# Kernel tuning notes

Hardware: AMD Instinct MI355X
Metric: run time of the kernel (lower is better)

Reference implementation:

```python
import jax, jax.numpy as jnp
import numpy as np

B, T, F = 256, 2048, 20
H_NODES = 256


def _heaviside(x):
    # smooth heaviside approx used throughout the original module
    return (jnp.tanh(10.0 * x) + 1.0) * 0.5


def _evap(wu, wl, wd, pet):
    h = _heaviside
    et1 = h(wu - pet) * pet + h(pet - wu) * wu
    rp = h(pet - et1) * (pet - et1)  # h(-(pet-et1))*0 term vanishes
    et22 = h(rp - wl) * wl + h(wl - rp) * rp
    et2 = h(rp) * et22
    et33 = h(rp - et2 - wd) * wd + h(wd - (rp - et2)) * (rp - et2)
    et3 = h(rp - et2) * et33
    return et1, et2, et3


def _runoff(wu, wl, wd, p, wum, wlm, wdm, b, c):
    wum = wum * 19.9 + 0.1
    wlm = wlm * 30.0 + 60.0
    wdm = wdm * 60.0 + 60.0
    c = c * 0.19 + 0.01
    b = b * 0.3 + 0.1
    w_total = wum + wlm + wdm
    s = c * (wu / w_total) ** 2 + b * (wl / w_total) ** 2
    return _heaviside(p - s) * (p - s)


def _partition(runoff, k1, k2, k3):
    k1 = k1 * 0.69 + 0.01
    k2 = k2 * 0.69 + 0.01
    k3 = k3 * 0.89 + 0.01
    sr = k1 * runoff
    itf = k2 * (runoff - sr)
    bf = k3 * (runoff - sr - itf)
    return sr, itf, bf


def setup_inputs() -> dict:
    key = jax.random.key(0)
    ks = jax.random.split(key, 7)
    u = lambda k, shp: jax.random.uniform(k, shp, jnp.float32, -0.05, 0.05)
    inputs = jax.random.uniform(ks[0], (B, T, F), jnp.float32)
    return {
        "inputs": inputs,
        "w1": u(ks[1], (15, H_NODES)),
        "b1": jnp.zeros((H_NODES,), jnp.float32),
        "w2": u(ks[2], (H_NODES, 64)),
        "b2": jnp.zeros((64,), jnp.float32),
        "w3": u(ks[3], (64, 8)),
        "b3": jnp.zeros((8,), jnp.float32),
    }


def reference(inputs, w1, b1, w2, b2, w3, b3):
    pet = inputs[..., 0:1]
    tmean = inputs[..., 1:2]
    p = inputs[..., 2:3]
    attrs = inputs[..., 5:]  # [B,T,15]

    # static-attribute -> physical-parameter MLP
    h1 = jnp.tanh(attrs @ w1 + b1)
    h2 = jnp.tanh(h1 @ w2 + b2)
    params = jax.nn.sigmoid(h2 @ w3 + b3)  # [B,T,8]

    xs = jnp.concatenate([pet, p, tmean, params], axis=-1)  # [B,T,11]

    def step(state, x):
        wu, wl, wd = state[:, 0:1], state[:, 1:2], state[:, 2:3]
        pet_t, p_t = x[:, 0:1], x[:, 1:2]
        et1, et2, et3 = _evap(wu, wl, wd, pet_t)
        clip = lambda d: jnp.clip(d, -1e5, 1e5)
        wu_n = wu + clip(p_t - et1)
        wl_n = wl + clip(p_t - et1 - et2)
        wd_n = wd + clip(p_t - et1 - et2 - et3)
        ns = jnp.concatenate([wu_n, wl_n, wd_n], axis=1)  # [B,3]
        return ns, ns

    init = jnp.zeros((inputs.shape[0], 3), inputs.dtype)
    _, outs = jax.lax.scan(step, init, jnp.swapaxes(xs, 0, 1))  # [T,B,3]
    outputs = jnp.swapaxes(outs, 0, 1)  # [B,T,3]

    wu, wl, wd = outputs[..., 0:1], outputs[..., 1:2], outputs[..., 2:3]
    wum, wlm, wdm = params[..., 0:1], params[..., 1:2], params[..., 2:3]
    b, c = params[..., 3:4], params[..., 4:5]
    k1, k2, k3 = params[..., 5:6], params[..., 6:7], params[..., 7:8]

    et1, et2, et3 = _evap(wu, wl, wd, pet)
    # NOTE: original call() swaps (wl,wd) and (wlm,wdm) here - kept faithful
    runoff = _runoff(wu, wd, wl, p, wum, wdm, wlm, b, c)
    sr, itf, bf = _partition(runoff, k1, k2, k3)
    total_q = sr + itf * 0.5 + bf * 0.25  # flow routing
    return total_q  # [B,T,1]
```

## Files before the change

### kernel.cpp

```cpp
#include <hip/hip_runtime.h>

#define B_ 256
#define T_ 2048
#define F_ 20
#define NT (B_*T_)

typedef __bf16 bf16x8 __attribute__((ext_vector_type(8)));
typedef float  f32x4  __attribute__((ext_vector_type(4)));

__device__ __forceinline__ float ex2(float x){ return __builtin_amdgcn_exp2f(x); }
__device__ __forceinline__ float rcpf_(float x){ return __builtin_amdgcn_rcpf(x); }

#define K10F 28.853900817779268f
#define K1F   2.8853900817779268f
#define LOG2E 1.4426950408889634f

__device__ __forceinline__ float hside(float x){ return 1.0f - rcpf_(ex2(K10F*x) + 1.0f); }
__device__ __forceinline__ float tanh_f(float z){ return 1.0f - 2.0f*rcpf_(ex2(K1F*z) + 1.0f); }
__device__ __forceinline__ float sigmoid_f(float z){ return rcpf_(1.0f + ex2(-LOG2E*z)); }


__global__ __launch_bounds__(256) void prep_kernel(const float* __restrict__ in,
                                                   float* __restrict__ ws){
  int r = blockIdx.x*256 + threadIdx.x;
  if (r >= NT) return;
  int b = r & (B_-1);
  int t = r >> 8;
  const float* src = in + ((size_t)b*T_ + t)*F_;
  ((float2*)ws)[r] = make_float2(src[0], src[2]);
}

__global__ __launch_bounds__(512) void fused_kernel(const float* __restrict__ in,
    const float* __restrict__ w1, const float* __restrict__ b1,
    const float* __restrict__ w2, const float* __restrict__ b2,
    const float* __restrict__ w3, const float* __restrict__ b3,
    float* __restrict__ ws){
  extern __shared__ char sm[];
  float* pk4 = ws + 4*(size_t)NT;

  if (blockIdx.x < 4) {
    asm volatile("s_setprio 3");
    const float2* pp2 = (const float2*)ws;
    float* wuT = ws + 2*(size_t)NT;
    float* wdT = ws + 3*(size_t)NT;
    float2* abL = (float2*)sm;
    float2* qbL = (float2*)(sm + 32768);

    int tid = threadIdx.x;
    int wv = tid >> 6, lane = tid & 63;
    int boff = blockIdx.x * 64;

    float wu = 0.0f, wl = 0.0f, wd = 0.0f;
    float2 buf[2][8];

    if (wv == 0){
      #pragma unroll
      for (int i = 0; i < 8; ++i){
        buf[0][i] = pp2[(    i)*B_ + boff + lane];
        buf[1][i] = pp2[(8 + i)*B_ + boff + lane];
      }
    }

    for (int it = 0; it < 66; ++it){
      if (wv == 0){
        if (it < 64){
          int c = it, par = c & 1;
          #pragma unroll
          for (int g = 0; g < 4; ++g){
            #pragma unroll
            for (int i = 0; i < 8; ++i){
              int s = g*8 + i;
              float pet = buf[g&1][i].x, p = buf[g&1][i].y;
              float d  = wu - pet;
              float r1 = rcpf_(ex2(K10F*d) + 1.0f);
              float d1 = -d*r1;
              float base = (p - pet) + d1;
              wu += base;
              wuT[(c*32 + s)*B_ + boff + lane] = wu;
              float r2 = rcpf_(ex2(K10F*d1) + 1.0f);
              float rp = fmaf(-d1, r2, d1);
              abL[(par*32 + s)*64 + lane] = make_float2(rp, base);
            }
            int gn = c*4 + g + 2;
            if (gn > 255) gn = 255;
            #pragma unroll
            for (int i = 0; i < 8; ++i)
              buf[g&1][i] = pp2[(gn*8 + i)*B_ + boff + lane];
          }
        }
      } else if (wv == 1){
        if (it >= 1 && it <= 64){
          int c = it - 1, par = c & 1;
          #pragma unroll 1
          for (int half = 0; half < 2; ++half){
            #pragma unroll
            for (int s0 = 0; s0 < 16; ++s0){
              int s = half*16 + s0;
              float2 ab  = abL[(par*32 + s)*64 + lane];
              float rp   = ab.x, base = ab.y;
              float hrp  = 1.0f - rcpf_(ex2(K10F*rp) + 1.0f);
              float d2   = rp - wl;
              float r    = rcpf_(ex2(K10F*d2) + 1.0f);
              float et22 = fmaf(d2, r, wl);
              float et2  = hrp * et22;
              float b2v  = base - et2;
              wl += b2v;
              qbL[(par*32 + s)*64 + lane] = make_float2(rp - et2, b2v);
            }
          }
        }
      } else if (wv == 2){
        if (it >= 2){
          int c = it - 2, par = c & 1;
          #pragma unroll 1
          for (int half = 0; half < 2; ++half){
            #pragma unroll
            for (int s0 = 0; s0 < 16; ++s0){
              int s = half*16 + s0;
              float2 qb  = qbL[(par*32 + s)*64 + lane];
              float hqv  = 1.0f - rcpf_(ex2(K10F*qb.x) + 1.0f);
              float d3   = qb.x - wd;
              float r    = rcpf_(ex2(K10F*d3) + 1.0f);
              float et33 = fmaf(d3, r, wd);
              float et3  = hqv * et33;
              wd += qb.y - et3;
              wdT[(c*32 + s)*B_ + boff + lane] = wd;
            }
          }
        }
      }
      __syncthreads();
    }
    return;
  }

  __bf16* w1f   = (__bf16*)sm;
  __bf16* w2f   = (__bf16*)(sm + 8192);
  float*  b1s   = (float*)(sm + 24576);
  float*  b2s   = (float*)(sm + 25600);
  float*  b3s   = (float*)(sm + 25856);
  __bf16* hbufA = (__bf16*)(sm + 25888);

  int tid  = threadIdx.x;
  int lane = tid & 63;
  int wv   = tid >> 6;
  int m    = lane & 15;
  int q    = lane >> 4;
  int r0   = (blockIdx.x - 4)*256 + wv*32;

  bf16x8 a1[2];
  #pragma unroll
  for (int u = 0; u < 2; ++u){
    int rowA = r0 + u*16 + m;
    int bA = rowA & (B_-1), tA = rowA >> 8;
    const float* ap = in + ((size_t)bA*T_ + tA)*F_ + 5;
    #pragma unroll
    for (int j = 0; j < 8; ++j){
      int k = q*8 + j;
      a1[u][j] = (__bf16)((k < 15) ? ap[k] : 0.0f);
    }
  }
  bf16x8 w3h[2], w3l[2];
  #pragma unroll
  for (int kb = 0; kb < 2; ++kb){
    #pragma unroll
    for (int j = 0; j < 8; ++j){
      float v = (m < 8) ? w3[(kb*32 + q*8 + j)*8 + m] : 0.0f;
      __bf16 hi = (__bf16)v;
      w3h[kb][j] = hi;
      w3l[kb][j] = (__bf16)(v - (float)hi);
    }
  }

  ((float4*)sm)[tid] = make_float4(0.0f, 0.0f, 0.0f, 0.0f);
  __syncthreads();
  for (int idx = tid; idx < 15*256; idx += 512){
    int k = idx >> 8, n = idx & 255;
    int ct = n >> 4;
    int l  = ((k>>3)*16) + (n & 15);
    int j  = k & 7;
    w1f[(ct*32 + l)*8 + j] = (__bf16)w1[idx];
  }
  for (int idx = tid; idx < 8192; idx += 512){
    int kk = idx >> 6, n = idx & 63;
    int kb2 = kk >> 5;
    int lq  = (kk >> 3) & 3;
    int j   = kk & 7;
    int ct  = n >> 4;
    int l   = lq*16 + (n & 15);
    w2f[((kb2*4 + ct)*64 + l)*8 + j] = (__bf16)w2[kk*64 + n];
  }
  if (tid < 256) b1s[tid] = b1[tid];
  if (tid < 64)  b2s[tid] = b2[tid];
  if (tid < 8)   b3s[tid] = b3[tid];
  __syncthreads();

  f32x4 zero4 = {0.0f, 0.0f, 0.0f, 0.0f};
  bf16x8 zero8;
  #pragma unroll
  for (int j = 0; j < 8; ++j) zero8[j] = (__bf16)0.0f;

  __bf16* hb = hbufA + wv*2304;
  f32x4 acc2[2][4] = {{zero4, zero4, zero4, zero4},
                      {zero4, zero4, zero4, zero4}};

  #pragma unroll
  for (int pc = 0; pc < 2; ++pc){
    if (pc == 1){
      __syncthreads();
      for (int idx = tid; idx < 8192; idx += 512){
        int kk = idx >> 6, n = idx & 63;
        int kb2 = kk >> 5;
        int lq  = (kk >> 3) & 3;
        int j   = kk & 7;
        int ct  = n >> 4;
        int l   = lq*16 + (n & 15);
        w2f[((kb2*4 + ct)*64 + l)*8 + j] = (__bf16)w2[(128 + kk)*64 + n];
      }
      __syncthreads();
    }
    #pragma unroll
    for (int ph = 0; ph < 2; ++ph){
      int p = pc*2 + ph;
      #pragma unroll
      for (int c4 = 0; c4 < 4; ++c4){
        int ct = p*4 + c4;
        bf16x8 bw = zero8;
        if (lane < 32) bw = *(const bf16x8*)&w1f[(ct*32 + lane)*8];
        int f = c4*16 + m;
        float bb = b1s[p*64 + f];
        #pragma unroll
        for (int u = 0; u < 2; ++u){
          f32x4 c1 = __builtin_amdgcn_mfma_f32_16x16x32_bf16(a1[u], bw, zero4, 0, 0, 0);
          #pragma unroll
          for (int i = 0; i < 4; ++i){
            float h = tanh_f(c1[i] + bb);
            hb[(u*16 + q*4 + i)*72 + f] = (__bf16)h;
          }
        }
      }
      #pragma unroll
      for (int kb = 0; kb < 2; ++kb){
        bf16x8 a2_0 = *(const bf16x8*)&hb[ m      *72 + kb*32 + q*8];
        bf16x8 a2_1 = *(const bf16x8*)&hb[(16 + m)*72 + kb*32 + q*8];
        #pragma unroll
        for (int ct = 0; ct < 4; ++ct){
          bf16x8 bw2 = *(const bf16x8*)&w2f[(((ph*2 + kb)*4 + ct)*64 + lane)*8];
          acc2[0][ct] = __builtin_amdgcn_mfma_f32_16x16x32_bf16(a2_0, bw2, acc2[0][ct], 0, 0, 0);
          acc2[1][ct] = __builtin_amdgcn_mfma_f32_16x16x32_bf16(a2_1, bw2, acc2[1][ct], 0, 0, 0);
        }
      }
    }
  }

  #pragma unroll
  for (int ct = 0; ct < 4; ++ct){
    int f = ct*16 + m;
    float bb = b2s[f];
    #pragma unroll
    for (int u = 0; u < 2; ++u)
      #pragma unroll
      for (int i = 0; i < 4; ++i){
        float h = tanh_f(acc2[u][ct][i] + bb);
        hb[(u*16 + q*4 + i)*72 + f] = (__bf16)h;
      }
  }

  f32x4 acc3[2] = {zero4, zero4};
  #pragma unroll
  for (int kb = 0; kb < 2; ++kb){
    bf16x8 a3_0 = *(const bf16x8*)&hb[ m      *72 + kb*32 + q*8];
    bf16x8 a3_1 = *(const bf16x8*)&hb[(16 + m)*72 + kb*32 + q*8];
    acc3[0] = __builtin_amdgcn_mfma_f32_16x16x32_bf16(a3_0, w3h[kb], acc3[0], 0, 0, 0);
    acc3[0] = __builtin_amdgcn_mfma_f32_16x16x32_bf16(a3_0, w3l[kb], acc3[0], 0, 0, 0);
    acc3[1] = __builtin_amdgcn_mfma_f32_16x16x32_bf16(a3_1, w3h[kb], acc3[1], 0, 0, 0);
    acc3[1] = __builtin_amdgcn_mfma_f32_16x16x32_bf16(a3_1, w3l[kb], acc3[1], 0, 0, 0);
  }

  float* hf = (float*)hb;
  if (m < 8){
    float bb3 = b3s[m];
    #pragma unroll
    for (int u = 0; u < 2; ++u)
      #pragma unroll
      for (int i = 0; i < 4; ++i)
        hf[(u*16 + q*4 + i)*9 + m] = sigmoid_f(acc3[u][i] + bb3);
  }
  if (lane < 32){
    const float* Pr = hf + lane*9;
    float P0=Pr[0], P1=Pr[1], P2=Pr[2], P3=Pr[3];
    float P4=Pr[4], P5=Pr[5], P6=Pr[6], P7=Pr[7];
    float wum = fmaf(P0, 19.9f, 0.1f);
    float wlm = fmaf(P2, 30.0f, 60.0f);
    float wdm = fmaf(P1, 60.0f, 60.0f);
    float wt  = wum + wlm + wdm;
    float rw  = 1.0f / wt;
    float cc  = fmaf(P4, 0.19f, 0.01f);
    float bc  = fmaf(P3, 0.30f, 0.10f);
    float A   = cc*rw*rw;
    float Bc  = bc*rw*rw;
    float k1  = fmaf(P5, 0.69f, 0.01f);
    float k2  = fmaf(P6, 0.69f, 0.01f);
    float k3  = fmaf(P7, 0.89f, 0.01f);
    float KP  = k1 + 0.5f*k2*(1.0f-k1) + 0.25f*k3*(1.0f-k1)*(1.0f-k2);
    *(float4*)&pk4[(size_t)(r0 + lane)*4] = make_float4(A, Bc, KP, 0.0f);
  }
}

__global__ __launch_bounds__(256) void final_kernel(const float* __restrict__ ws,
                                                    float* __restrict__ out){
  __shared__ float tile[64*65];
  int tb = blockIdx.x & 31;
  int bb = blockIdx.x >> 5;
  int t0 = tb*64, b0 = bb*64;
  int tid = threadIdx.x;
  const float2* pp2 = (const float2*)ws;
  const float* wuT  = ws + 2*(size_t)NT;
  const float* wdT  = ws + 3*(size_t)NT;
  const float* pk4  = ws + 4*(size_t)NT;

  #pragma unroll
  for (int k = 0; k < 16; ++k){
    int idx = k*256 + tid;
    int tl = idx >> 6, bl = idx & 63;
    int r = (t0 + tl)*B_ + b0 + bl;
    float p  = pp2[r].y;
    float wu = wuT[r], wd = wdT[r];
    float4 k4 = *(const float4*)&pk4[(size_t)r*4];
    float ps = p - k4.x*wu*wu - k4.y*wd*wd;
    float runoff = hside(ps)*ps;
    tile[bl*65 + tl] = k4.z * runoff;
  }
  __syncthreads();
  #pragma unroll
  for (int k = 0; k < 16; ++k){
    int idx = k*256 + tid;
    int tl2 = idx & 63, bl2 = idx >> 6;
    out[(size_t)(b0 + bl2)*T_ + t0 + tl2] = tile[bl2*65 + tl2];
  }
}

extern "C" void kernel_launch(void* const* d_in, const int* in_sizes, int n_in,
                              void* d_out, int out_size, void* d_ws, size_t ws_size,
                              hipStream_t stream) {
  const float* in = (const float*)d_in[0];
  const float* w1 = (const float*)d_in[1];
  const float* b1 = (const float*)d_in[2];
  const float* w2 = (const float*)d_in[3];
  const float* b2 = (const float*)d_in[4];
  const float* w3 = (const float*)d_in[5];
  const float* b3 = (const float*)d_in[6];
  float* out = (float*)d_out;
  float* ws  = (float*)d_ws;

  static bool attr_set = false;
  if (!attr_set){
    hipFuncSetAttribute((const void*)fused_kernel,
                        hipFuncAttributeMaxDynamicSharedMemorySize, 65536);
    attr_set = true;
  }

  prep_kernel <<<NT/256,     256, 0,     stream>>>(in, ws);
  fused_kernel<<<NT/256 + 4, 512, 65536, stream>>>(in, w1, b1, w2, b2, w3, b3, ws);
  final_kernel<<<128,        256, 0,     stream>>>(ws, out);
}
```

Baseline: 221.6 us.

## Move recurrent scan into prep kernel and read forcings directly from input

The sequential three-store scan moves out of the fused MLP kernel and into the prep kernel, as 4 extra blocks that run alongside the transpose blocks. The scan wave now loads pet and p straight from the original input with float4 loads and a deeper 4-group prefetch, instead of reading the transposed workspace. This removes the scan's dependence on the prep pass and frees the MLP kernel from hosting long-running scan blocks. The cost is that the scan no longer overlaps the MLP, which now starts only after the scan finishes. The per-lane loads are also strided across batch rows and poorly coalesced.

Result: slower. 388.0 us (+75.1%).

```diff
diff --git a/kernel.cpp b/kernel.cpp
--- a/kernel.cpp
+++ b/kernel.cpp
@@ -20,17 +20,113 @@
 __device__ __forceinline__ float sigmoid_f(float z){ return rcpf_(1.0f + ex2(-LOG2E*z)); }
 
 
-__global__ __launch_bounds__(256) void prep_kernel(const float* __restrict__ in,
-                                                   float* __restrict__ ws){
-  int r = blockIdx.x*256 + threadIdx.x;
-  if (r >= NT) return;
-  int b = r & (B_-1);
-  int t = r >> 8;
-  const float* src = in + ((size_t)b*T_ + t)*F_;
-  ((float2*)ws)[r] = make_float2(src[0], src[2]);
+__global__ __launch_bounds__(256) void scan_prep_kernel(const float* __restrict__ in,
+                                                        float* __restrict__ ws){
+  extern __shared__ char sm[];
+
+  if (blockIdx.x >= 4){
+    int r = (blockIdx.x - 4)*256 + threadIdx.x;
+    int b = r & (B_-1);
+    int t = r >> 8;
+    const float* src = in + ((size_t)b*T_ + t)*F_;
+    ((float2*)ws)[r] = make_float2(src[0], src[2]);
+    return;
+  }
+
+  float* wuT = ws + 2*(size_t)NT;
+  float* wdT = ws + 3*(size_t)NT;
+  float2* abL = (float2*)sm;
+  float2* qbL = (float2*)(sm + 32768);
+
+  int tid = threadIdx.x;
+  int wv = tid >> 6, lane = tid & 63;
+  int boff = blockIdx.x * 64;
+  const float* bp = in + (size_t)(boff + lane)*T_*F_;
+
+  float wu = 0.0f, wl = 0.0f, wd = 0.0f;
+  float4 buf[4][8];
+
+  if (wv == 0){
+    #pragma unroll
+    for (int g = 0; g < 4; ++g)
+      #pragma unroll
+      for (int i = 0; i < 8; ++i)
+        buf[g][i] = *(const float4*)(bp + (size_t)(g*8 + i)*F_);
+  }
+
+  for (int it = 0; it < 66; ++it){
+    if (wv == 0){
+      if (it < 64){
+        int c = it, par = c & 1;
+        #pragma unroll
+        for (int g = 0; g < 4; ++g){
+          #pragma unroll
+          for (int i = 0; i < 8; ++i){
+            int s = g*8 + i;
+            float pet = buf[g][i].x, p = buf[g][i].z;
+            float d  = wu - pet;
+            float r1 = rcpf_(ex2(K10F*d) + 1.0f);
+            float d1 = -d*r1;
+            float base = (p - pet) + d1;
+            wu += base;
+            wuT[(c*32 + s)*B_ + boff + lane] = wu;
+            float r2 = rcpf_(ex2(K10F*d1) + 1.0f);
+            float rp = fmaf(-d1, r2, d1);
+            abL[(par*32 + s)*64 + lane] = make_float2(rp, base);
+          }
+          int gn = c*4 + g + 4;
+          if (gn > 255) gn = 255;
+          #pragma unroll
+          for (int i = 0; i < 8; ++i)
+            buf[g][i] = *(const float4*)(bp + (size_t)(gn*8 + i)*F_);
+        }
+      }
+    } else if (wv == 1){
+      if (it >= 1 && it <= 64){
+        int c = it - 1, par = c & 1;
+        #pragma unroll 1
+        for (int half = 0; half < 2; ++half){
+          #pragma unroll
+          for (int s0 = 0; s0 < 16; ++s0){
+            int s = half*16 + s0;
+            float2 ab  = abL[(par*32 + s)*64 + lane];
+            float rp   = ab.x, base = ab.y;
+            float hrp  = 1.0f - rcpf_(ex2(K10F*rp) + 1.0f);
+            float d2   = rp - wl;
+            float r    = rcpf_(ex2(K10F*d2) + 1.0f);
+            float et22 = fmaf(d2, r, wl);
+            float et2  = hrp * et22;
+            float b2v  = base - et2;
+            wl += b2v;
+            qbL[(par*32 + s)*64 + lane] = make_float2(rp - et2, b2v);
+          }
+        }
+      }
+    } else if (wv == 2){
+      if (it >= 2){
+        int c = it - 2, par = c & 1;
+        #pragma unroll 1
+        for (int half = 0; half < 2; ++half){
+          #pragma unroll
+          for (int s0 = 0; s0 < 16; ++s0){
+            int s = half*16 + s0;
+            float2 qb  = qbL[(par*32 + s)*64 + lane];
+            float hqv  = 1.0f - rcpf_(ex2(K10F*qb.x) + 1.0f);
+            float d3   = qb.x - wd;
+            float r    = rcpf_(ex2(K10F*d3) + 1.0f);
+            float et33 = fmaf(d3, r, wd);
+            float et3  = hqv * et33;
+            wd += qb.y - et3;
+            wdT[(c*32 + s)*B_ + boff + lane] = wd;
+          }
+        }
+      }
+    }
+    __syncthreads();
+  }
 }
 
-__global__ __launch_bounds__(512) void fused_kernel(const float* __restrict__ in,
+__global__ __launch_bounds__(512) void mlp_kernel(const float* __restrict__ in,
     const float* __restrict__ w1, const float* __restrict__ b1,
     const float* __restrict__ w2, const float* __restrict__ b2,
     const float* __restrict__ w3, const float* __restrict__ b3,
@@ -38,102 +134,6 @@
   extern __shared__ char sm[];
   float* pk4 = ws + 4*(size_t)NT;
 
-  if (blockIdx.x < 4) {
-    asm volatile("s_setprio 3");
-    const float2* pp2 = (const float2*)ws;
-    float* wuT = ws + 2*(size_t)NT;
-    float* wdT = ws + 3*(size_t)NT;
-    float2* abL = (float2*)sm;
-    float2* qbL = (float2*)(sm + 32768);
-
-    int tid = threadIdx.x;
-    int wv = tid >> 6, lane = tid & 63;
-    int boff = blockIdx.x * 64;
-
-    float wu = 0.0f, wl = 0.0f, wd = 0.0f;
-    float2 buf[2][8];
-
-    if (wv == 0){
-      #pragma unroll
-      for (int i = 0; i < 8; ++i){
-        buf[0][i] = pp2[(    i)*B_ + boff + lane];
-        buf[1][i] = pp2[(8 + i)*B_ + boff + lane];
-      }
-    }
-
-    for (int it = 0; it < 66; ++it){
-      if (wv == 0){
-        if (it < 64){
-          int c = it, par = c & 1;
-          #pragma unroll
-          for (int g = 0; g < 4; ++g){
-            #pragma unroll
-            for (int i = 0; i < 8; ++i){
-              int s = g*8 + i;
-              float pet = buf[g&1][i].x, p = buf[g&1][i].y;
-              float d  = wu - pet;
-              float r1 = rcpf_(ex2(K10F*d) + 1.0f);
-              float d1 = -d*r1;
-              float base = (p - pet) + d1;
-              wu += base;
-              wuT[(c*32 + s)*B_ + boff + lane] = wu;
-              float r2 = rcpf_(ex2(K10F*d1) + 1.0f);
-              float rp = fmaf(-d1, r2, d1);
-              abL[(par*32 + s)*64 + lane] = make_float2(rp, base);
-            }
-            int gn = c*4 + g + 2;
-            if (gn > 255) gn = 255;
-            #pragma unroll
-            for (int i = 0; i < 8; ++i)
-              buf[g&1][i] = pp2[(gn*8 + i)*B_ + boff + lane];
-          }
-        }
-      } else if (wv == 1){
-        if (it >= 1 && it <= 64){
-          int c = it - 1, par = c & 1;
-          #pragma unroll 1
-          for (int half = 0; half < 2; ++half){
-            #pragma unroll
-            for (int s0 = 0; s0 < 16; ++s0){
-              int s = half*16 + s0;
-              float2 ab  = abL[(par*32 + s)*64 + lane];
-              float rp   = ab.x, base = ab.y;
-              float hrp  = 1.0f - rcpf_(ex2(K10F*rp) + 1.0f);
-              float d2   = rp - wl;
-              float r    = rcpf_(ex2(K10F*d2) + 1.0f);
-              float et22 = fmaf(d2, r, wl);
-              float et2  = hrp * et22;
-              float b2v  = base - et2;
-              wl += b2v;
-              qbL[(par*32 + s)*64 + lane] = make_float2(rp - et2, b2v);
-            }
-          }
-        }
-      } else if (wv == 2){
-        if (it >= 2){
-          int c = it - 2, par = c & 1;
-          #pragma unroll 1
-          for (int half = 0; half < 2; ++half){
-            #pragma unroll
-            for (int s0 = 0; s0 < 16; ++s0){
-              int s = half*16 + s0;
-              float2 qb  = qbL[(par*32 + s)*64 + lane];
-              float hqv  = 1.0f - rcpf_(ex2(K10F*qb.x) + 1.0f);
-              float d3   = qb.x - wd;
-              float r    = rcpf_(ex2(K10F*d3) + 1.0f);
-              float et33 = fmaf(d3, r, wd);
-              float et3  = hqv * et33;
-              wd += qb.y - et3;
-              wdT[(c*32 + s)*B_ + boff + lane] = wd;
-            }
-          }
-        }
-      }
-      __syncthreads();
-    }
-    return;
-  }
-
   __bf16* w1f   = (__bf16*)sm;
   __bf16* w2f   = (__bf16*)(sm + 8192);
   float*  b1s   = (float*)(sm + 24576);
@@ -146,7 +146,7 @@
   int wv   = tid >> 6;
   int m    = lane & 15;
   int q    = lane >> 4;
-  int r0   = (blockIdx.x - 4)*256 + wv*32;
+  int r0   = blockIdx.x*256 + wv*32;
 
   bf16x8 a1[2];
   #pragma unroll
@@ -355,12 +355,12 @@
 
   static bool attr_set = false;
   if (!attr_set){
-    hipFuncSetAttribute((const void*)fused_kernel,
+    hipFuncSetAttribute((const void*)scan_prep_kernel,
                         hipFuncAttributeMaxDynamicSharedMemorySize, 65536);
     attr_set = true;
   }
 
-  prep_kernel <<<NT/256,     256, 0,     stream>>>(in, ws);
-  fused_kernel<<<NT/256 + 4, 512, 65536, stream>>>(in, w1, b1, w2, b2, w3, b3, ws);
-  final_kernel<<<128,        256, 0,     stream>>>(ws, out);
+  scan_prep_kernel<<<2052, 256, 65536, stream>>>(in, ws);
+  mlp_kernel      <<<2048, 512, 62752, stream>>>(in, w1, b1, w2, b2, w3, b3, ws);
+  final_kernel    <<<128,  256, 0,     stream>>>(ws, out);
 }
```
